# Performance work log

Measured on AMD Instinct MI355X. Metric: run time of the kernel, lower is better.

Reference implementation:

```python
import jax, jax.numpy as jnp
import numpy as np

N = 8192        # total nodes
E = 131072      # total edges (avg degree 16)
G = 32          # graphs
F = 64          # hidden channel multiplicity
T = 2           # num_interactions
D = 128         # readout (output_irreps) dim per interaction
NUM_EL = 5
R_MAX = 2.03
NBASIS = 8
NUM_RADII = 64          # len(arange(0.75, 2.03, 0.02))
POS_LM = 16             # (position_coeffs_lmax+1)^2 = 16
SH_DIM = 9              # (max_ell+1)^2 with max_ell=2
AVG_NEIGH = 16.0
L_IDX = jnp.array([0, 1, 1, 1, 2, 2, 2, 2, 2])  # which l each SH component belongs to


def _sph_harm(u):
    # real spherical harmonics up to l=2 on unit vectors u: [E,3] -> [E,9]
    x, y, z = u[:, 0], u[:, 1], u[:, 2]
    c1 = np.sqrt(3.0); c2 = np.sqrt(15.0); c3 = np.sqrt(5.0) / 2.0
    return jnp.stack([
        jnp.ones_like(x),
        c1 * x, c1 * y, c1 * z,
        c2 * x * y, c2 * y * z, c3 * (3.0 * z * z - 1.0), c2 * x * z,
        (c2 / 2.0) * (x * x - y * y),
    ], axis=-1)


def setup_inputs() -> dict:
    key = jax.random.key(0)
    ks = jax.random.split(key, 18)
    positions = jax.random.uniform(ks[0], (N, 3), dtype=jnp.float32) * 1.5
    species = jax.random.randint(ks[1], (N,), 0, NUM_EL)
    senders = jax.random.randint(ks[2], (E,), 0, N)
    receivers = jax.random.randint(ks[3], (E,), 0, N)
    n_node = jnp.full((G,), N // G, dtype=jnp.int32)
    target_species = jax.random.randint(ks[4], (G,), 0, NUM_EL)

    def rn(k, shape, fan):
        return (jax.random.normal(k, shape, dtype=jnp.float32) / np.sqrt(fan)).astype(jnp.float32)

    params = dict(
        emb_table=rn(ks[5], (NUM_EL, F), 1.0),
        W1=rn(ks[6], (T, NBASIS, 64), NBASIS),
        W2=rn(ks[7], (T, 64, F * 3), 64),
        W_self=rn(ks[8], (T, F, F), F),
        W_upd=rn(ks[9], (T, F, F), F),
        W_read=rn(ks[10], (T, F * SH_DIM, D), F * SH_DIM),
        w_focus=rn(ks[11], (T * D,), T * D),
        Ws1=rn(ks[12], (T * D, 128), T * D),
        Ws2=rn(ks[13], (128, NUM_EL), 128),
        species_table=rn(ks[14], (NUM_EL, T * D), 1.0),
        W_pos=rn(ks[15], (T * D, NUM_RADII * POS_LM), T * D),
    )
    return dict(positions=positions, species=species, senders=senders,
                receivers=receivers, n_node=n_node, target_species=target_species,
                **params)


def reference(positions, species, senders, receivers, n_node, target_species,
              emb_table, W1, W2, W_self, W_upd, W_read, w_focus, Ws1, Ws2,
              species_table, W_pos):
    # edge geometry
    vec = positions[receivers] - positions[senders]          # [E,3]
    d = jnp.linalg.norm(vec, axis=-1)
    d_safe = jnp.maximum(d, 1e-9)
    Y = _sph_harm(vec / d_safe[:, None])                      # [E,9]
    # bessel radial basis (8 functions) with soft envelope
    n = jnp.arange(1, NBASIS + 1, dtype=jnp.float32)
    basis = np.sqrt(2.0 / R_MAX) * jnp.sin(n[None, :] * jnp.pi * d_safe[:, None] / R_MAX) / d_safe[:, None]
    tt = jnp.clip(d / R_MAX, 0.0, 1.0 - 1e-6)
    env = jnp.where(d < R_MAX, jnp.exp(-tt * tt / (1.0 - tt * tt)), 0.0)  # [E]

    x = emb_table[species]                                    # [N,F] scalar features
    reads = []
    for li in range(T):
        h = jax.nn.softplus(basis @ W1[li]) @ W2[li] * env[:, None]   # [E, F*3]
        Rw = h.reshape(E, F, 3)[:, :, L_IDX]                          # [E,F,9] per-l weight
        msg = x[senders][:, :, None] * Y[:, None, :] * Rw             # [E,F,9]
        agg = jax.ops.segment_sum(msg, receivers, num_segments=N) / AVG_NEIGH  # [N,F,9]
        reads.append(agg.reshape(N, F * SH_DIM) @ W_read[li])         # [N,D]
        x = jax.nn.silu(agg[:, :, 0] @ W_upd[li] + x @ W_self[li])    # scalar update

    emb = jnp.concatenate(reads, axis=-1)                     # [N, T*D]
    focus_logits = emb @ w_focus                              # [N]
    first_idx = jnp.concatenate([jnp.zeros(1, jnp.int32),
                                 jnp.cumsum(n_node)[:-1].astype(jnp.int32)])
    femb = emb[first_idx]                                     # [G, T*D]
    species_logits = jax.nn.softplus(femb @ Ws1) @ Ws2        # [G,5]
    pos = ((species_table[target_species] * femb) @ W_pos).reshape(G, NUM_RADII, POS_LM)
    return focus_logits, species_logits, pos
```

## Files before the change

### kernel.cpp

```cpp
#include <hip/hip_runtime.h>
#include <hip/hip_bf16.h>

#define NN 8192
#define EE 131072
#define GG 32
#define FF 64
#define DDIM 128
#define NB 8
#define SH 9
#define RMAX 2.03f
#define INV_AVG (1.0f/16.0f)

typedef __attribute__((ext_vector_type(8))) short short8v;
typedef __attribute__((ext_vector_type(4))) float float4v;

__device__ __forceinline__ float softplus_f(float v){
  float t = exp2f(v*1.44269504f);
  float r = 0.69314718f*log2f(1.0f+t);
  return (v > 80.0f) ? v : r;
}
__device__ __forceinline__ unsigned short f2bf(float f){
  __hip_bfloat16 h = __float2bfloat16(f);
  return *reinterpret_cast<unsigned short*>(&h);
}
__device__ __forceinline__ float bf2f(unsigned short h){
  return __uint_as_float(((unsigned int)h)<<16);
}

__global__ __launch_bounds__(256) void k_deg(const int* __restrict__ rcv, int* __restrict__ deg)
{
  int e = blockIdx.x*256 + threadIdx.x;
  if (e < EE) atomicAdd(&deg[rcv[e]], 1);
}

__global__ __launch_bounds__(256) void k_scan(const int* __restrict__ deg,
                                              int* __restrict__ off, int* __restrict__ cur)
{
  __shared__ int part[256];
  int t = threadIdx.x;
  int base = t*32;
  int s = 0;
  for (int i=0;i<32;i++) s += deg[base+i];
  part[t] = s;
  __syncthreads();
  for (int o2=1;o2<256;o2<<=1){
    int v = (t>=o2)? part[t-o2] : 0;
    __syncthreads();
    part[t] += v;
    __syncthreads();
  }
  int run = part[t]-s;
  for (int i=0;i<32;i++){
    off[base+i]=run; cur[base+i]=run;
    run += deg[base+i];
  }
  if (t==255) off[NN]=run;
}

__global__ __launch_bounds__(256) void k_fill(const int* __restrict__ rcv,
                                              int* __restrict__ cur, int* __restrict__ eidx)
{
  int e = blockIdx.x*256 + threadIdx.x;
  if (e < EE){
    int p = atomicAdd(&cur[rcv[e]], 1);
    eidx[p] = e;
  }
}

__global__ __launch_bounds__(256) void k_prep(
    const float* __restrict__ pos, const int* __restrict__ snd, const int* __restrict__ rcv,
    const int* __restrict__ eidx, const int* __restrict__ spec, const float* __restrict__ et,
    float* __restrict__ Yb, float* __restrict__ Bb, float* __restrict__ Eb,
    int* __restrict__ snds, float* __restrict__ x)
{
  int b = blockIdx.x;
  if (b < 512){
    int j = b*256 + threadIdx.x;
    int e = eidx[j];
    int s = snd[e], r = rcv[e];
    snds[j] = s;
    float dx = pos[3*r  ]-pos[3*s  ];
    float dy = pos[3*r+1]-pos[3*s+1];
    float dz = pos[3*r+2]-pos[3*s+2];
    float d  = sqrtf(dx*dx+dy*dy+dz*dz);
    float dsafe = fmaxf(d, 1e-9f);
    float inv = 1.0f/dsafe;
    float xx = dx*inv, yy = dy*inv, zz = dz*inv;
    const float c1=1.7320508075688772f, c2=3.872983346207417f, c3=1.118033988749895f;
    float Y[SH];
    Y[0]=1.0f; Y[1]=c1*xx; Y[2]=c1*yy; Y[3]=c1*zz;
    Y[4]=c2*xx*yy; Y[5]=c2*yy*zz; Y[6]=c3*(3.0f*zz*zz-1.0f); Y[7]=c2*xx*zz; Y[8]=0.5f*c2*(xx*xx-yy*yy);
    #pragma unroll
    for (int i=0;i<SH;i++) Yb[(size_t)j*SH+i]=Y[i];
    float sc = sqrtf(2.0f/RMAX)*inv;
    float th = 3.14159265358979f*dsafe/RMAX;
    float s1 = sinf(th), cth = cosf(th);
    float skm = 0.0f, sk = s1, twoc = 2.0f*cth;
    #pragma unroll
    for (int k=0;k<NB;k++){
      Bb[(size_t)j*NB+k] = sc*sk;
      float sn = twoc*sk - skm;
      skm = sk; sk = sn;
    }
    float tt = fminf(d/RMAX, 1.0f-1e-6f);
    Eb[j] = (d < RMAX) ? exp2f(-1.44269504f*tt*tt/(1.0f-tt*tt)) : 0.0f;
  } else {
    int i0 = ((b-512)*256 + threadIdx.x)*8;
    int n = i0 >> 6, f0 = i0 & 63;
    const float4v* src = (const float4v*)(et + (size_t)spec[n]*FF + f0);
    float4v v0 = src[0], v1 = src[1];
    *(float4v*)(x+i0)   = v0;
    *(float4v*)(x+i0+4) = v1;
  }
}

__global__ __launch_bounds__(256) void k_pack(
    const float* __restrict__ W2, const float* __restrict__ Wr,
    unsigned short* __restrict__ Bp, unsigned short* __restrict__ Wrp)
{
  int b = blockIdx.x;
  if (b < 96){
    int id = b*256 + threadIdx.x;
    int j  = id & 7;
    int l  = (id>>3) & 63;
    int s  = (id>>9) & 1;
    int rem = id >> 10;
    int t  = rem % 12;
    int li = rem / 12;
    int k  = s*32 + (l>>4)*8 + j;
    int colp = t*16 + (l&15);
    int f = colp & 63, c = colp >> 6;
    Bp[id] = f2bf(W2[(size_t)li*FF*192 + k*192 + 3*f + c]);
  } else {
    int id = (b-96)*256 + threadIdx.x;
    int j  = id & 7;
    int l  = (id>>3) & 63;
    int t  = (id>>9) & 7;
    int rem = id >> 12;
    int ks = rem % 18;
    int li = rem / 18;
    int k  = ks*32 + (l>>4)*8 + j;
    int col = t*16 + (l&15);
    Wrp[id] = f2bf(Wr[(size_t)li*576*DDIM + k*DDIM + col]);
  }
}

__global__ __launch_bounds__(256) void k_gemm2s(
    const float* __restrict__ Bb, const float* __restrict__ Eb,
    const float* __restrict__ W1l, const unsigned short* __restrict__ Bpl,
    unsigned short* __restrict__ O)
{
  __shared__ float sW1[NB*FF];
  __shared__ unsigned short sO[4][16*200];
  int tid = threadIdx.x;
  for (int i=tid;i<NB*FF;i+=256) sW1[i]=W1l[i];
  __syncthreads();

  int lane = tid & 63, wv = tid >> 6;
  int r0 = (blockIdx.x*4 + wv) * 16;
  int mrow = lane & 15, kg = lane >> 4;

  const float4v* bp = (const float4v*)(Bb + (size_t)(r0 + mrow)*NB);
  float4v b0v = bp[0], b1v = bp[1];
  float B8[8] = {b0v[0],b0v[1],b0v[2],b0v[3],b1v[0],b1v[1],b1v[2],b1v[3]};
  float es = Eb[r0 + mrow]*INV_AVG;

  short8v a0, a1;
  #pragma unroll
  for (int j=0;j<8;j++){
    int kc = kg*8 + j;
    float h0=0.0f, h1=0.0f;
    #pragma unroll
    for (int b=0;b<NB;b++){
      h0 += B8[b]*sW1[b*FF + kc];
      h1 += B8[b]*sW1[b*FF + kc + 32];
    }
    a0[j] = (short)f2bf(softplus_f(h0)*es);
    a1[j] = (short)f2bf(softplus_f(h1)*es);
  }

  unsigned short* myO = sO[wv];
  #pragma unroll
  for (int t=0;t<12;t++){
    short8v b0 = *(const short8v*)(Bpl + ((size_t)(t*2+0)*64 + lane)*8);
    short8v b1 = *(const short8v*)(Bpl + ((size_t)(t*2+1)*64 + lane)*8);
    float4v acc = {0.0f,0.0f,0.0f,0.0f};
    acc = __builtin_amdgcn_mfma_f32_16x16x32_bf16(a0, b0, acc, 0, 0, 0);
    acc = __builtin_amdgcn_mfma_f32_16x16x32_bf16(a1, b1, acc, 0, 0, 0);
    #pragma unroll
    for (int i=0;i<4;i++)
      myO[(kg*4+i)*200 + t*16 + mrow] = f2bf(acc[i]);
  }

  const size_t tbase = (size_t)r0*192;
  #pragma unroll
  for (int it=0; it<6; ++it){
    int F = it*512 + lane*8;
    int r = F/192, c = F - r*192;
    short8v v = *(const short8v*)&myO[r*200 + c];
    *(short8v*)(O + tbase + F) = v;
  }
}

__global__ __launch_bounds__(256) void k_gather2(
  const float* __restrict__ Yb, const int* __restrict__ snds, const int* __restrict__ off,
  const float* __restrict__ x, const unsigned short* __restrict__ O,
  unsigned short* __restrict__ aggb, float* __restrict__ c0)
{
  int lane = threadIdx.x & 63, wv = threadIdx.x >> 6;
  int n = blockIdx.x*4 + wv;
  int js = off[n], je = off[n+1];
  float acc[SH];
  #pragma unroll
  for (int i=0;i<SH;i++) acc[i]=0.0f;
  for (int j=js;j<je;j++){
    const unsigned short* orow = O + (size_t)j*192;
    float o0 = bf2f(orow[lane]);
    float o1 = bf2f(orow[64+lane]);
    float o2 = bf2f(orow[128+lane]);
    float xs = x[(size_t)snds[j]*FF + lane];
    const float* y = Yb + (size_t)j*SH;
    float p0=o0*xs, p1=o1*xs, p2=o2*xs;
    acc[0]+=y[0]*p0;
    acc[1]+=y[1]*p1; acc[2]+=y[2]*p1; acc[3]+=y[3]*p1;
    acc[4]+=y[4]*p2; acc[5]+=y[5]*p2; acc[6]+=y[6]*p2;
    acc[7]+=y[7]*p2; acc[8]+=y[8]*p2;
  }
  unsigned short* db = aggb + (size_t)n*576 + lane*SH;
  #pragma unroll
  for (int i=0;i<SH;i++) db[i]=f2bf(acc[i]);
  c0[(size_t)n*FF + lane] = acc[0];
}

__global__ __launch_bounds__(128) void k_read_mfma(
    const unsigned short* __restrict__ aggb, const unsigned short* __restrict__ Wrpl,
    float* __restrict__ emb, int colOff)
{
  int tid = threadIdx.x;
  int lane = tid & 63, wv = tid >> 6;
  int r0 = (blockIdx.x*2 + wv)*16;
  int mrow = lane & 15, kgrp = lane >> 4;
  float4v acc[8];
  #pragma unroll
  for (int t=0;t<8;t++){ acc[t][0]=0.f; acc[t][1]=0.f; acc[t][2]=0.f; acc[t][3]=0.f; }
  const unsigned short* arow = aggb + (size_t)(r0+mrow)*576 + kgrp*8;
  #pragma unroll 3
  for (int ks=0; ks<18; ++ks){
    short8v a = *(const short8v*)(arow + ks*32);
    #pragma unroll
    for (int t=0;t<8;t++){
      short8v b = *(const short8v*)(Wrpl + (((size_t)ks*8+t)*64 + lane)*8);
      acc[t] = __builtin_amdgcn_mfma_f32_16x16x32_bf16(a, b, acc[t], 0, 0, 0);
    }
  }
  #pragma unroll
  for (int t=0;t<8;t++){
    #pragma unroll
    for (int i=0;i<4;i++){
      emb[(size_t)(r0 + kgrp*4 + i)*256 + colOff + t*16 + mrow] = acc[t][i];
    }
  }
}

__global__ __launch_bounds__(256) void k_upd(
    const float* __restrict__ c0, const float* __restrict__ xin,
    const float* __restrict__ Wu, const float* __restrict__ Wsf, float* __restrict__ xout)
{
  __shared__ float sWu[FF*FF], sWs[FF*FF];
  __shared__ float sA[4][FF], sX[4][FF];
  int t = threadIdx.x;
  for (int i=t;i<FF*FF;i+=256){ sWu[i]=Wu[i]; sWs[i]=Wsf[i]; }
  int lane = t&63, wv = t>>6;
  int n = blockIdx.x*4 + wv;
  sA[wv][lane] = c0[(size_t)n*FF + lane];
  sX[wv][lane] = xin[n*FF + lane];
  __syncthreads();
  float a=0.0f;
  #pragma unroll 8
  for (int k=0;k<FF;k++) a += sA[wv][k]*sWu[k*FF+lane] + sX[wv][k]*sWs[k*FF+lane];
  float sg = 1.0f/(1.0f+exp2f(-1.44269504f*a));
  xout[n*FF+lane] = a*sg;
}

__global__ __launch_bounds__(256) void k_heads(
    const float* __restrict__ emb, const float* __restrict__ wf,
    const int* __restrict__ nnode, const int* __restrict__ tspec,
    const float* __restrict__ Ws1, const float* __restrict__ Ws2,
    const float* __restrict__ stab, const float* __restrict__ Wpos,
    float* __restrict__ outF, float* __restrict__ outSp, float* __restrict__ outPos)
{
  int b = blockIdx.x, t = threadIdx.x;
  if (b < 2048){
    int lane = t&63, wv = t>>6;
    int n = b*4 + wv;
    float a=0.0f;
    #pragma unroll
    for (int j=0;j<4;j++) a += emb[(size_t)n*256 + j*64 + lane]*wf[j*64+lane];
    #pragma unroll
    for (int off=32; off>0; off>>=1) a += __shfl_down(a, off, 64);
    if (lane==0) outF[n]=a;
  } else if (b < 2080){
    __shared__ float sf[256], sh2[128];
    int g = b - 2048;
    int fi = 0;
    for (int i=0;i<g;i++) fi += nnode[i];
    sf[t] = emb[(size_t)fi*256 + t];
    __syncthreads();
    if (t < 128){
      float a=0.0f;
      #pragma unroll 4
      for (int k=0;k<256;k++) a += sf[k]*Ws1[k*128+t];
      sh2[t] = softplus_f(a);
    }
    __syncthreads();
    if (t < 5){
      float a=0.0f;
      for (int k=0;k<128;k++) a += sh2[k]*Ws2[k*5+t];
      outSp[g*5+t]=a;
    }
  } else {
    __shared__ float ssp[256];
    int pb = b - 2080;
    int g = pb >> 2;
    int p = (pb & 3)*256 + t;
    int fi = 0;
    for (int i=0;i<g;i++) fi += nnode[i];
    int ts = tspec[g];
    ssp[t] = emb[(size_t)fi*256 + t]*stab[(size_t)ts*256 + t];
    __syncthreads();
    float a=0.0f;
    #pragma unroll 4
    for (int k=0;k<256;k++) a += ssp[k]*Wpos[(size_t)k*1024 + p];
    outPos[(size_t)g*1024 + p] = a;
  }
}

extern "C" void kernel_launch(void* const* d_in, const int* in_sizes, int n_in,
                              void* d_out, int out_size, void* d_ws, size_t ws_size,
                              hipStream_t stream)
{
  const float* positions = (const float*)d_in[0];
  const int*   species   = (const int*)  d_in[1];
  const int*   senders   = (const int*)  d_in[2];
  const int*   receivers = (const int*)  d_in[3];
  const int*   n_node    = (const int*)  d_in[4];
  const int*   tspec     = (const int*)  d_in[5];
  const float* emb_table = (const float*)d_in[6];
  const float* W1        = (const float*)d_in[7];
  const float* W2        = (const float*)d_in[8];
  const float* W_self    = (const float*)d_in[9];
  const float* W_upd     = (const float*)d_in[10];
  const float* W_read    = (const float*)d_in[11];
  const float* w_focus   = (const float*)d_in[12];
  const float* Ws1       = (const float*)d_in[13];
  const float* Ws2       = (const float*)d_in[14];
  const float* stab      = (const float*)d_in[15];
  const float* W_pos     = (const float*)d_in[16];

  char* base = (char*)d_ws;
  size_t ofs = 0;
  auto alloc = [&](size_t bytes)->char*{
    char* p = base + ofs;
    ofs = (ofs + bytes + 255) & ~(size_t)255;
    return p;
  };
  float* Yb   = (float*)alloc((size_t)EE*SH*4);
  float* Bb   = (float*)alloc((size_t)EE*NB*4);
  float* Eb   = (float*)alloc((size_t)EE*4);
  int*   snds = (int*)  alloc((size_t)EE*4);
  float* xA   = (float*)alloc((size_t)NN*FF*4);
  float* xB   = (float*)alloc((size_t)NN*FF*4);
  float* c0   = (float*)alloc((size_t)NN*FF*4);
  float* emb  = (float*)alloc((size_t)NN*256*4);
  int*   deg  = (int*)  alloc((size_t)NN*4);
  int*   off  = (int*)  alloc((size_t)(NN+1)*4);
  int*   cur  = (int*)  alloc((size_t)NN*4);
  int*   eidx = (int*)  alloc((size_t)EE*4);
  unsigned short* O    = (unsigned short*)alloc((size_t)EE*192*2);
  unsigned short* aggb = (unsigned short*)alloc((size_t)NN*576*2);
  unsigned short* Bp   = (unsigned short*)alloc((size_t)2*12*2*64*8*2);
  unsigned short* Wrp  = (unsigned short*)alloc((size_t)2*18*8*64*8*2);

  float* outFocus = (float*)d_out;
  float* outSp    = outFocus + NN;
  float* outPos   = outSp + GG*5;

  (void)hipMemsetAsync(deg, 0, NN*sizeof(int), stream);
  k_deg<<<EE/256,256,0,stream>>>(receivers,deg);
  k_scan<<<1,256,0,stream>>>(deg,off,cur);
  k_fill<<<EE/256,256,0,stream>>>(receivers,cur,eidx);
  k_prep<<<768,256,0,stream>>>(positions,senders,receivers,eidx,species,emb_table,
                               Yb,Bb,Eb,snds,xA);
  k_pack<<<672,256,0,stream>>>(W2,W_read,Bp,Wrp);

  k_gemm2s<<<EE/64,256,0,stream>>>(Bb,Eb,W1,Bp,O);
  k_gather2<<<NN/4,256,0,stream>>>(Yb,snds,off,xA,O,aggb,c0);
  k_read_mfma<<<NN/32,128,0,stream>>>(aggb,Wrp,emb,0);
  k_upd<<<NN/4,256,0,stream>>>(c0,xA,W_upd,W_self,xB);

  k_gemm2s<<<EE/64,256,0,stream>>>(Bb,Eb,W1+NB*FF,Bp+(size_t)12*2*64*8,O);
  k_gather2<<<NN/4,256,0,stream>>>(Yb,snds,off,xB,O,aggb,c0);
  k_read_mfma<<<NN/32,128,0,stream>>>(aggb,Wrp+(size_t)18*8*64*8,emb,DDIM);

  k_heads<<<2208,256,0,stream>>>(emb,w_focus,n_node,tspec,Ws1,Ws2,stab,W_pos,
                                 outFocus,outSp,outPos);
}
```

Before: 277.2 us.

## Fuse radial MLP MFMA GEMM with per-node edge gather aggregation

Merges the per-edge radial weight GEMM (k_gemm2s) and the receiver-sorted gather (k_gather2) into one kernel. Each wave processes its node's incoming edges in chunks of 16, computes the radial weights with MFMA in registers, and multiplies them directly by sender features and spherical harmonics. The partial sums across the four k-groups are combined with cross-lane shuffles. This removes the E×192 bf16 intermediate buffer and its write and read round trip. In exchange, tiles for low-degree nodes are partially padded, MFMA work is wasted on those rows, and register pressure rises from the 36 accumulators.

```diff
diff --git a/kernel.cpp b/kernel.cpp
--- a/kernel.cpp
+++ b/kernel.cpp
@@ -145,91 +145,119 @@
   }
 }
 
-__global__ __launch_bounds__(256) void k_gemm2s(
-    const float* __restrict__ Bb, const float* __restrict__ Eb,
-    const float* __restrict__ W1l, const unsigned short* __restrict__ Bpl,
-    unsigned short* __restrict__ O)
+__global__ __launch_bounds__(256) void k_fused2(
+  const float* __restrict__ Bb, const float* __restrict__ Eb, const float* __restrict__ Yb,
+  const int* __restrict__ snds, const int* __restrict__ off,
+  const float* __restrict__ x, const float* __restrict__ W1l,
+  const unsigned short* __restrict__ Bpl,
+  unsigned short* __restrict__ aggb, float* __restrict__ c0)
 {
   __shared__ float sW1[NB*FF];
-  __shared__ unsigned short sO[4][16*200];
+  __shared__ float sStage[4][580];
   int tid = threadIdx.x;
   for (int i=tid;i<NB*FF;i+=256) sW1[i]=W1l[i];
   __syncthreads();
 
   int lane = tid & 63, wv = tid >> 6;
-  int r0 = (blockIdx.x*4 + wv) * 16;
-  int mrow = lane & 15, kg = lane >> 4;
-
-  const float4v* bp = (const float4v*)(Bb + (size_t)(r0 + mrow)*NB);
-  float4v b0v = bp[0], b1v = bp[1];
-  float B8[8] = {b0v[0],b0v[1],b0v[2],b0v[3],b1v[0],b1v[1],b1v[2],b1v[3]};
-  float es = Eb[r0 + mrow]*INV_AVG;
-
-  short8v a0, a1;
-  #pragma unroll
-  for (int j=0;j<8;j++){
-    int kc = kg*8 + j;
-    float h0=0.0f, h1=0.0f;
-    #pragma unroll
-    for (int b=0;b<NB;b++){
-      h0 += B8[b]*sW1[b*FF + kc];
-      h1 += B8[b]*sW1[b*FF + kc + 32];
-    }
-    a0[j] = (short)f2bf(softplus_f(h0)*es);
-    a1[j] = (short)f2bf(softplus_f(h1)*es);
-  }
-
-  unsigned short* myO = sO[wv];
-  #pragma unroll
-  for (int t=0;t<12;t++){
-    short8v b0 = *(const short8v*)(Bpl + ((size_t)(t*2+0)*64 + lane)*8);
-    short8v b1 = *(const short8v*)(Bpl + ((size_t)(t*2+1)*64 + lane)*8);
-    float4v acc = {0.0f,0.0f,0.0f,0.0f};
-    acc = __builtin_amdgcn_mfma_f32_16x16x32_bf16(a0, b0, acc, 0, 0, 0);
-    acc = __builtin_amdgcn_mfma_f32_16x16x32_bf16(a1, b1, acc, 0, 0, 0);
-    #pragma unroll
-    for (int i=0;i<4;i++)
-      myO[(kg*4+i)*200 + t*16 + mrow] = f2bf(acc[i]);
-  }
-
-  const size_t tbase = (size_t)r0*192;
-  #pragma unroll
-  for (int it=0; it<6; ++it){
-    int F = it*512 + lane*8;
-    int r = F/192, c = F - r*192;
-    short8v v = *(const short8v*)&myO[r*200 + c];
-    *(short8v*)(O + tbase + F) = v;
-  }
-}
-
-__global__ __launch_bounds__(256) void k_gather2(
-  const float* __restrict__ Yb, const int* __restrict__ snds, const int* __restrict__ off,
-  const float* __restrict__ x, const unsigned short* __restrict__ O,
-  unsigned short* __restrict__ aggb, float* __restrict__ c0)
-{
-  int lane = threadIdx.x & 63, wv = threadIdx.x >> 6;
   int n = blockIdx.x*4 + wv;
   int js = off[n], je = off[n+1];
-  float acc[SH];
+  int mrow = lane & 15, kg = lane >> 4;
+
+  float acc[4][9];
   #pragma unroll
-  for (int i=0;i<SH;i++) acc[i]=0.0f;
-  for (int j=js;j<je;j++){
-    const unsigned short* orow = O + (size_t)j*192;
-    float o0 = bf2f(orow[lane]);
-    float o1 = bf2f(orow[64+lane]);
-    float o2 = bf2f(orow[128+lane]);
-    float xs = x[(size_t)snds[j]*FF + lane];
-    const float* y = Yb + (size_t)j*SH;
-    float p0=o0*xs, p1=o1*xs, p2=o2*xs;
-    acc[0]+=y[0]*p0;
-    acc[1]+=y[1]*p1; acc[2]+=y[2]*p1; acc[3]+=y[3]*p1;
-    acc[4]+=y[4]*p2; acc[5]+=y[5]*p2; acc[6]+=y[6]*p2;
-    acc[7]+=y[7]*p2; acc[8]+=y[8]*p2;
-  }
+  for (int fg=0;fg<4;fg++)
+    #pragma unroll
+    for (int q=0;q<9;q++) acc[fg][q]=0.0f;
+
+  for (int t0 = js; t0 < je; t0 += 16){
+    int row = t0 + mrow;
+    bool v = row < je;
+    float B8[8];
+    float es = 0.0f;
+    if (v){
+      const float4v* bp = (const float4v*)(Bb + (size_t)row*NB);
+      float4v b0v = bp[0], b1v = bp[1];
+      B8[0]=b0v[0];B8[1]=b0v[1];B8[2]=b0v[2];B8[3]=b0v[3];
+      B8[4]=b1v[0];B8[5]=b1v[1];B8[6]=b1v[2];B8[7]=b1v[3];
+      es = Eb[row]*INV_AVG;
+    } else {
+      #pragma unroll
+      for (int b=0;b<8;b++) B8[b]=0.0f;
+    }
+    short8v a0, a1;
+    #pragma unroll
+    for (int j=0;j<8;j++){
+      int kc = kg*8 + j;
+      float h0=0.0f, h1=0.0f;
+      #pragma unroll
+      for (int b=0;b<NB;b++){
+        h0 += B8[b]*sW1[b*FF + kc];
+        h1 += B8[b]*sW1[b*FF + kc + 32];
+      }
+      a0[j] = (short)f2bf(softplus_f(h0)*es);
+      a1[j] = (short)f2bf(softplus_f(h1)*es);
+    }
+    int rc[4];
+    float xv[4][4];
+    #pragma unroll
+    for (int i=0;i<4;i++){
+      int r2 = t0 + kg*4 + i;
+      rc[i] = (r2 < je) ? r2 : js;
+      int xs = snds[rc[i]];
+      #pragma unroll
+      for (int fg=0;fg<4;fg++) xv[i][fg] = x[(size_t)xs*FF + fg*16 + mrow];
+    }
+    #pragma unroll
+    for (int c=0;c<3;c++){
+      const int sh0 = (c==0)?0:(c==1)?1:4;
+      const int nsh = (c==0)?1:(c==1)?3:5;
+      float ys[4][5];
+      #pragma unroll
+      for (int i=0;i<4;i++){
+        const float* y = Yb + (size_t)rc[i]*SH;
+        #pragma unroll
+        for (int q=0;q<5;q++) ys[i][q] = (q<nsh) ? y[sh0+q] : 0.0f;
+      }
+      #pragma unroll
+      for (int fg=0;fg<4;fg++){
+        int t = c*4 + fg;
+        short8v b0 = *(const short8v*)(Bpl + ((size_t)(t*2+0)*64 + lane)*8);
+        short8v b1 = *(const short8v*)(Bpl + ((size_t)(t*2+1)*64 + lane)*8);
+        float4v o4 = {0.0f,0.0f,0.0f,0.0f};
+        o4 = __builtin_amdgcn_mfma_f32_16x16x32_bf16(a0, b0, o4, 0, 0, 0);
+        o4 = __builtin_amdgcn_mfma_f32_16x16x32_bf16(a1, b1, o4, 0, 0, 0);
+        #pragma unroll
+        for (int i=0;i<4;i++){
+          float p = o4[i]*xv[i][fg];
+          #pragma unroll
+          for (int q=0;q<5;q++)
+            if (q<nsh) acc[fg][sh0+q] += ys[i][q]*p;
+        }
+      }
+    }
+  }
+
+  #pragma unroll
+  for (int fg=0;fg<4;fg++)
+    #pragma unroll
+    for (int q=0;q<9;q++){
+      float vv = acc[fg][q];
+      vv += __shfl_xor(vv, 16, 64);
+      vv += __shfl_xor(vv, 32, 64);
+      acc[fg][q] = vv;
+    }
+  if (kg == 0){
+    #pragma unroll
+    for (int fg=0;fg<4;fg++)
+      #pragma unroll
+      for (int q=0;q<9;q++)
+        sStage[wv][(fg*16 + mrow)*9 + q] = acc[fg][q];
+  }
+  __syncthreads();
   unsigned short* db = aggb + (size_t)n*576 + lane*SH;
   #pragma unroll
-  for (int i=0;i<SH;i++) db[i]=f2bf(acc[i]);
-  c0[(size_t)n*FF + lane] = acc[0];
+  for (int q=0;q<9;q++) db[q] = f2bf(sStage[wv][lane*9 + q]);
+  c0[(size_t)n*FF + lane] = sStage[wv][lane*9];
 }
 
 __global__ __launch_bounds__(128) void k_read_mfma(
@@ -376,7 +404,6 @@
   int*   off  = (int*)  alloc((size_t)(NN+1)*4);
   int*   cur  = (int*)  alloc((size_t)NN*4);
   int*   eidx = (int*)  alloc((size_t)EE*4);
-  unsigned short* O    = (unsigned short*)alloc((size_t)EE*192*2);
   unsigned short* aggb = (unsigned short*)alloc((size_t)NN*576*2);
   unsigned short* Bp   = (unsigned short*)alloc((size_t)2*12*2*64*8*2);
   unsigned short* Wrp  = (unsigned short*)alloc((size_t)2*18*8*64*8*2);
@@ -393,13 +420,11 @@
                                Yb,Bb,Eb,snds,xA);
   k_pack<<<672,256,0,stream>>>(W2,W_read,Bp,Wrp);
 
-  k_gemm2s<<<EE/64,256,0,stream>>>(Bb,Eb,W1,Bp,O);
-  k_gather2<<<NN/4,256,0,stream>>>(Yb,snds,off,xA,O,aggb,c0);
+  k_fused2<<<NN/4,256,0,stream>>>(Bb,Eb,Yb,snds,off,xA,W1,Bp,aggb,c0);
   k_read_mfma<<<NN/32,128,0,stream>>>(aggb,Wrp,emb,0);
   k_upd<<<NN/4,256,0,stream>>>(c0,xA,W_upd,W_self,xB);
 
-  k_gemm2s<<<EE/64,256,0,stream>>>(Bb,Eb,W1+NB*FF,Bp+(size_t)12*2*64*8,O);
-  k_gather2<<<NN/4,256,0,stream>>>(Yb,snds,off,xB,O,aggb,c0);
+  k_fused2<<<NN/4,256,0,stream>>>(Bb,Eb,Yb,snds,off,xB,W1+NB*FF,Bp+(size_t)12*2*64*8,aggb,c0);
   k_read_mfma<<<NN/32,128,0,stream>>>(aggb,Wrp+(size_t)18*8*64*8,emb,DDIM);
 
   k_heads<<<2208,256,0,stream>>>(emb,w_focus,n_node,tspec,Ws1,Ws2,stab,W_pos,
```

Result: slower. 365.6 us (+31.9%).

## Replace per-edge radial MLP with distance-indexed lookup table and interpolation

Applied to the files above, without the earlier changes.

The radial network (basis, softplus MLP, envelope, W2 projection) depends only on edge distance. The per-edge bf16 MFMA GEMM and its large intermediate buffer are replaced by a 2049-entry per-interaction table precomputed over distance. The gather kernel now linearly interpolates table rows instead of reading a per-edge output row. This removes heavy per-edge compute and memory traffic, at the cost of interpolation error plus a table-build kernel where each block reloads W2 into shared memory.

```diff
diff --git a/kernel.cpp b/kernel.cpp
--- a/kernel.cpp
+++ b/kernel.cpp
@@ -10,6 +10,7 @@
 #define SH 9
 #define RMAX 2.03f
 #define INV_AVG (1.0f/16.0f)
+#define TABN 2048
 
 typedef __attribute__((ext_vector_type(8))) short short8v;
 typedef __attribute__((ext_vector_type(4))) float float4v;
@@ -70,7 +71,7 @@
 __global__ __launch_bounds__(256) void k_prep(
     const float* __restrict__ pos, const int* __restrict__ snd, const int* __restrict__ rcv,
     const int* __restrict__ eidx, const int* __restrict__ spec, const float* __restrict__ et,
-    float* __restrict__ Yb, float* __restrict__ Bb, float* __restrict__ Eb,
+    float* __restrict__ Yb, float* __restrict__ ub,
     int* __restrict__ snds, float* __restrict__ x)
 {
   int b = blockIdx.x;
@@ -92,18 +93,8 @@
     Y[4]=c2*xx*yy; Y[5]=c2*yy*zz; Y[6]=c3*(3.0f*zz*zz-1.0f); Y[7]=c2*xx*zz; Y[8]=0.5f*c2*(xx*xx-yy*yy);
     #pragma unroll
     for (int i=0;i<SH;i++) Yb[(size_t)j*SH+i]=Y[i];
-    float sc = sqrtf(2.0f/RMAX)*inv;
-    float th = 3.14159265358979f*dsafe/RMAX;
-    float s1 = sinf(th), cth = cosf(th);
-    float skm = 0.0f, sk = s1, twoc = 2.0f*cth;
-    #pragma unroll
-    for (int k=0;k<NB;k++){
-      Bb[(size_t)j*NB+k] = sc*sk;
-      float sn = twoc*sk - skm;
-      skm = sk; sk = sn;
-    }
-    float tt = fminf(d/RMAX, 1.0f-1e-6f);
-    Eb[j] = (d < RMAX) ? exp2f(-1.44269504f*tt*tt/(1.0f-tt*tt)) : 0.0f;
+    float u = fminf(d*((float)TABN/RMAX), 2047.999f);
+    ub[j] = u;
   } else {
     int i0 = ((b-512)*256 + threadIdx.x)*8;
     int n = i0 >> 6, f0 = i0 & 63;
@@ -115,96 +106,82 @@
 }
 
 __global__ __launch_bounds__(256) void k_pack(
-    const float* __restrict__ W2, const float* __restrict__ Wr,
-    unsigned short* __restrict__ Bp, unsigned short* __restrict__ Wrp)
-{
-  int b = blockIdx.x;
-  if (b < 96){
-    int id = b*256 + threadIdx.x;
-    int j  = id & 7;
-    int l  = (id>>3) & 63;
-    int s  = (id>>9) & 1;
-    int rem = id >> 10;
-    int t  = rem % 12;
-    int li = rem / 12;
-    int k  = s*32 + (l>>4)*8 + j;
-    int colp = t*16 + (l&15);
-    int f = colp & 63, c = colp >> 6;
-    Bp[id] = f2bf(W2[(size_t)li*FF*192 + k*192 + 3*f + c]);
-  } else {
-    int id = (b-96)*256 + threadIdx.x;
-    int j  = id & 7;
-    int l  = (id>>3) & 63;
-    int t  = (id>>9) & 7;
-    int rem = id >> 12;
-    int ks = rem % 18;
-    int li = rem / 18;
-    int k  = ks*32 + (l>>4)*8 + j;
-    int col = t*16 + (l&15);
-    Wrp[id] = f2bf(Wr[(size_t)li*576*DDIM + k*DDIM + col]);
-  }
-}
-
-__global__ __launch_bounds__(256) void k_gemm2s(
-    const float* __restrict__ Bb, const float* __restrict__ Eb,
-    const float* __restrict__ W1l, const unsigned short* __restrict__ Bpl,
-    unsigned short* __restrict__ O)
+    const float* __restrict__ Wr, unsigned short* __restrict__ Wrp)
+{
+  int id = blockIdx.x*256 + threadIdx.x;
+  int j  = id & 7;
+  int l  = (id>>3) & 63;
+  int t  = (id>>9) & 7;
+  int rem = id >> 12;
+  int ks = rem % 18;
+  int li = rem / 18;
+  int k  = ks*32 + (l>>4)*8 + j;
+  int col = t*16 + (l&15);
+  Wrp[id] = f2bf(Wr[(size_t)li*576*DDIM + k*DDIM + col]);
+}
+
+__global__ __launch_bounds__(256) void k_tab(
+    const float* __restrict__ W1, const float* __restrict__ W2,
+    unsigned short* __restrict__ Tb)
 {
   __shared__ float sW1[NB*FF];
-  __shared__ unsigned short sO[4][16*200];
-  int tid = threadIdx.x;
-  for (int i=tid;i<NB*FF;i+=256) sW1[i]=W1l[i];
+  __shared__ float sW2[FF*192];
+  __shared__ float sH[4][FF];
+  int li = blockIdx.x / 513;
+  int rb = (blockIdx.x % 513) * 4;
+  int tid = threadIdx.x, lane = tid & 63, wv = tid >> 6;
+  const float* W1l = W1 + li*NB*FF;
+  const float* W2l = W2 + (size_t)li*FF*192;
+  for (int i=tid;i<NB*FF;i+=256)  sW1[i]=W1l[i];
+  for (int i=tid;i<FF*192;i+=256) sW2[i]=W2l[i];
   __syncthreads();
 
-  int lane = tid & 63, wv = tid >> 6;
-  int r0 = (blockIdx.x*4 + wv) * 16;
-  int mrow = lane & 15, kg = lane >> 4;
-
-  const float4v* bp = (const float4v*)(Bb + (size_t)(r0 + mrow)*NB);
-  float4v b0v = bp[0], b1v = bp[1];
-  float B8[8] = {b0v[0],b0v[1],b0v[2],b0v[3],b1v[0],b1v[1],b1v[2],b1v[3]};
-  float es = Eb[r0 + mrow]*INV_AVG;
-
-  short8v a0, a1;
-  #pragma unroll
-  for (int j=0;j<8;j++){
-    int kc = kg*8 + j;
-    float h0=0.0f, h1=0.0f;
-    #pragma unroll
-    for (int b=0;b<NB;b++){
-      h0 += B8[b]*sW1[b*FF + kc];
-      h1 += B8[b]*sW1[b*FF + kc + 32];
-    }
-    a0[j] = (short)f2bf(softplus_f(h0)*es);
-    a1[j] = (short)f2bf(softplus_f(h1)*es);
-  }
-
-  unsigned short* myO = sO[wv];
-  #pragma unroll
-  for (int t=0;t<12;t++){
-    short8v b0 = *(const short8v*)(Bpl + ((size_t)(t*2+0)*64 + lane)*8);
-    short8v b1 = *(const short8v*)(Bpl + ((size_t)(t*2+1)*64 + lane)*8);
-    float4v acc = {0.0f,0.0f,0.0f,0.0f};
-    acc = __builtin_amdgcn_mfma_f32_16x16x32_bf16(a0, b0, acc, 0, 0, 0);
-    acc = __builtin_amdgcn_mfma_f32_16x16x32_bf16(a1, b1, acc, 0, 0, 0);
-    #pragma unroll
-    for (int i=0;i<4;i++)
-      myO[(kg*4+i)*200 + t*16 + mrow] = f2bf(acc[i]);
-  }
-
-  const size_t tbase = (size_t)r0*192;
-  #pragma unroll
-  for (int it=0; it<6; ++it){
-    int F = it*512 + lane*8;
-    int r = F/192, c = F - r*192;
-    short8v v = *(const short8v*)&myO[r*200 + c];
-    *(short8v*)(O + tbase + F) = v;
-  }
-}
-
-__global__ __launch_bounds__(256) void k_gather2(
-  const float* __restrict__ Yb, const int* __restrict__ snds, const int* __restrict__ off,
-  const float* __restrict__ x, const unsigned short* __restrict__ O,
+  int row = rb + wv;
+  bool valid = (row <= TABN);
+  int rowc = valid ? row : TABN;
+  float d = (float)rowc * (RMAX/(float)TABN);
+  float dsafe = fmaxf(d, 1e-9f);
+  float inv = 1.0f/dsafe;
+  float sc = sqrtf(2.0f/RMAX)*inv;
+  float th = 3.14159265358979f*dsafe/RMAX;
+  float s1 = sinf(th), cth = cosf(th);
+  float basis[NB];
+  {
+    float skm = 0.0f, sk = s1, twoc = 2.0f*cth;
+    #pragma unroll
+    for (int k=0;k<NB;k++){
+      basis[k] = sc*sk;
+      float sn = twoc*sk - skm;
+      skm = sk; sk = sn;
+    }
+  }
+  float tt = fminf(d/RMAX, 1.0f-1e-6f);
+  float env = (d < RMAX) ? exp2f(-1.44269504f*tt*tt/(1.0f-tt*tt)) : 0.0f;
+  float h = 0.0f;
+  #pragma unroll
+  for (int b=0;b<NB;b++) h += basis[b]*sW1[b*FF + lane];
+  sH[wv][lane] = softplus_f(h)*env*INV_AVG;
+  __syncthreads();
+
+  float o0=0.0f, o1=0.0f, o2=0.0f;
+  #pragma unroll 8
+  for (int k=0;k<FF;k++){
+    float hk = sH[wv][k];
+    const float* w = &sW2[k*192 + 3*lane];
+    o0 += hk*w[0]; o1 += hk*w[1]; o2 += hk*w[2];
+  }
+  if (valid){
+    unsigned short* dst = Tb + ((size_t)li*(TABN+1) + row)*192;
+    dst[lane]       = f2bf(o0);
+    dst[64 + lane]  = f2bf(o1);
+    dst[128 + lane] = f2bf(o2);
+  }
+}
+
+__global__ __launch_bounds__(256) void k_gath(
+  const float* __restrict__ Yb, const float* __restrict__ ub,
+  const int* __restrict__ snds, const int* __restrict__ off,
+  const float* __restrict__ x, const unsigned short* __restrict__ Tl,
   unsigned short* __restrict__ aggb, float* __restrict__ c0)
 {
   int lane = threadIdx.x & 63, wv = threadIdx.x >> 6;
@@ -214,10 +191,16 @@
   #pragma unroll
   for (int i=0;i<SH;i++) acc[i]=0.0f;
   for (int j=js;j<je;j++){
-    const unsigned short* orow = O + (size_t)j*192;
-    float o0 = bf2f(orow[lane]);
-    float o1 = bf2f(orow[64+lane]);
-    float o2 = bf2f(orow[128+lane]);
+    float u = ub[j];
+    int i = (int)u;
+    float f = u - (float)i;
+    const unsigned short* r = Tl + (size_t)i*192;
+    float a0 = bf2f(r[lane]),     b0v = bf2f(r[192+lane]);
+    float a1 = bf2f(r[64+lane]),  b1v = bf2f(r[256+lane]);
+    float a2 = bf2f(r[128+lane]), b2v = bf2f(r[320+lane]);
+    float o0 = a0 + f*(b0v-a0);
+    float o1 = a1 + f*(b1v-a1);
+    float o2 = a2 + f*(b2v-a2);
     float xs = x[(size_t)snds[j]*FF + lane];
     const float* y = Yb + (size_t)j*SH;
     float p0=o0*xs, p1=o1*xs, p2=o2*xs;
@@ -365,8 +348,7 @@
     return p;
   };
   float* Yb   = (float*)alloc((size_t)EE*SH*4);
-  float* Bb   = (float*)alloc((size_t)EE*NB*4);
-  float* Eb   = (float*)alloc((size_t)EE*4);
+  float* ub   = (float*)alloc((size_t)EE*4);
   int*   snds = (int*)  alloc((size_t)EE*4);
   float* xA   = (float*)alloc((size_t)NN*FF*4);
   float* xB   = (float*)alloc((size_t)NN*FF*4);
@@ -376,9 +358,8 @@
   int*   off  = (int*)  alloc((size_t)(NN+1)*4);
   int*   cur  = (int*)  alloc((size_t)NN*4);
   int*   eidx = (int*)  alloc((size_t)EE*4);
-  unsigned short* O    = (unsigned short*)alloc((size_t)EE*192*2);
   unsigned short* aggb = (unsigned short*)alloc((size_t)NN*576*2);
-  unsigned short* Bp   = (unsigned short*)alloc((size_t)2*12*2*64*8*2);
+  unsigned short* Tb   = (unsigned short*)alloc((size_t)2*(TABN+1)*192*2);
   unsigned short* Wrp  = (unsigned short*)alloc((size_t)2*18*8*64*8*2);
 
   float* outFocus = (float*)d_out;
@@ -390,16 +371,15 @@
   k_scan<<<1,256,0,stream>>>(deg,off,cur);
   k_fill<<<EE/256,256,0,stream>>>(receivers,cur,eidx);
   k_prep<<<768,256,0,stream>>>(positions,senders,receivers,eidx,species,emb_table,
-                               Yb,Bb,Eb,snds,xA);
-  k_pack<<<672,256,0,stream>>>(W2,W_read,Bp,Wrp);
-
-  k_gemm2s<<<EE/64,256,0,stream>>>(Bb,Eb,W1,Bp,O);
-  k_gather2<<<NN/4,256,0,stream>>>(Yb,snds,off,xA,O,aggb,c0);
+                               Yb,ub,snds,xA);
+  k_pack<<<576,256,0,stream>>>(W_read,Wrp);
+  k_tab<<<1026,256,0,stream>>>(W1,W2,Tb);
+
+  k_gath<<<NN/4,256,0,stream>>>(Yb,ub,snds,off,xA,Tb,aggb,c0);
   k_read_mfma<<<NN/32,128,0,stream>>>(aggb,Wrp,emb,0);
   k_upd<<<NN/4,256,0,stream>>>(c0,xA,W_upd,W_self,xB);
 
-  k_gemm2s<<<EE/64,256,0,stream>>>(Bb,Eb,W1+NB*FF,Bp+(size_t)12*2*64*8,O);
-  k_gather2<<<NN/4,256,0,stream>>>(Yb,snds,off,xB,O,aggb,c0);
+  k_gath<<<NN/4,256,0,stream>>>(Yb,ub,snds,off,xB,Tb+(size_t)(TABN+1)*192,aggb,c0);
   k_read_mfma<<<NN/32,128,0,stream>>>(aggb,Wrp+(size_t)18*8*64*8,emb,DDIM);
 
   k_heads<<<2208,256,0,stream>>>(emb,w_focus,n_node,tspec,Ws1,Ws2,stab,W_pos,
```

After: 253.6 us. 8.5% less time.
